# Optimization experiments

Measured on AMD Instinct MI355X. Metric: run time of the kernel, lower is better.

## Reference

```python
import jax, jax.numpy as jnp
import numpy as np

EPS = 1e-6  # VNLeakyReLU eps
NORM_EPS = 1e-12  # F.normalize default eps
NEG_SLOPE = 0.2


def _normalize(v):
    # matches torch F.normalize(p=2, dim=-1): v / max(||v||, eps)
    n = jnp.linalg.norm(v, axis=-1, keepdims=True)
    return v / jnp.maximum(n, NORM_EPS)


def _bgs_extended(d6s):
    # d6s: [B,N,D,3,2] -> rotation matrices [B,N,D,3,3] (columns b1,b2,b3)
    b1 = _normalize(d6s[..., 0])
    a2 = d6s[..., 1]
    proj = jnp.sum(b1 * a2, axis=-1, keepdims=True) * b1
    b2 = _normalize(a2 - proj)
    b3 = jnp.cross(b1, b2)
    return jnp.stack([b1, b2, b3], axis=-1)


def setup_inputs() -> dict:
    key = jax.random.key(0)
    kX, kJ, kA, kB, kC, kW = jax.random.split(key, 6)
    B, N, Din, Dout = 8, 4096, 128, 256
    return {
        "X": jax.random.normal(kX, (B, N, Din, 3), dtype=jnp.float32),
        "J": jax.random.normal(kJ, (B, N, Din, 3, 2), dtype=jnp.float32),
        "Amat": jax.random.normal(kA, (Dout, Din), dtype=jnp.float32),
        "Bmat": jax.random.normal(kB, (Dout, Din), dtype=jnp.float32),
        "Cmat": jax.random.normal(kC, (Dout, Din), dtype=jnp.float32),
        "Wdir": jax.random.normal(kW, (Dout, Dout), dtype=jnp.float32),
        "device": 0,
    }


def reference(X, J, Amat, Bmat, Cmat, Wdir, device):
    # ---- Affine_Linear_Abla_wocomplex ----
    R = _bgs_extended(J)  # [B,N,D,3,3]
    # get_rtx(k, RT, X) = sum_j R[...,j,k] * X[...,j]; stacking k=0,1,2 gives:
    a_term = jnp.einsum('bndjk,bndj->bndk', R, X)  # [B,N,D,3]
    # Y = A@a + B@a + C@a == (A+B+C)@a  (einsum 'fe,bcei->bcfi')
    Y = jnp.einsum('fe,bnei->bnfi', Amat + Bmat + Cmat, a_term)  # [B,N,F,3]
    # ---- permute(0,2,3,1) -> [B, F, 3, N] ----
    x = jnp.transpose(Y, (0, 2, 3, 1))
    # ---- VNLeakyReLU ----
    d = jnp.einsum('oc,bcin->boin', Wdir, x)
    dot = jnp.sum(x * d, axis=2, keepdims=True)
    mask = (dot >= 0).astype(x.dtype)
    d_norm_sq = jnp.sum(d * d, axis=2, keepdims=True)
    x_out = NEG_SLOPE * x + (1 - NEG_SLOPE) * (
        mask * x + (1 - mask) * (x - dot / (d_norm_sq + EPS) * d)
    )
    return x_out  # [B, F, 3, N]
```

## Files before the change

### kernel.cpp

```cpp
#include <hip/hip_runtime.h>

#define TT 16
#define NBLK 2048
#define LDA 136

typedef short s16x8 __attribute__((ext_vector_type(8)));
typedef float f32x4 __attribute__((ext_vector_type(4)));

#define SCHED_FENCE() __builtin_amdgcn_sched_barrier(0)

__device__ __forceinline__ unsigned short f2bf(float f) {
  union { float f; unsigned u; } v; v.f = f;
  unsigned r = v.u + 0x7FFFu + ((v.u >> 16) & 1u);
  return (unsigned short)(r >> 16);
}
__device__ __forceinline__ float bf2f(unsigned short h) {
  union { unsigned u; float f; } v; v.u = ((unsigned)h) << 16;
  return v.f;
}
__device__ __forceinline__ void split2(float x, unsigned short& h, unsigned short& m) {
  h = f2bf(x);
  m = f2bf(x - bf2f(h));
}

__global__ __launch_bounds__(256) void prep1_kernel(
    const float* __restrict__ A, const float* __restrict__ Bm,
    const float* __restrict__ C,
    float* __restrict__ M3f,
    unsigned short* __restrict__ M3h, unsigned short* __restrict__ M3m) {
  int tid = blockIdx.x * 256 + threadIdx.x;
  float s = A[tid] + Bm[tid] + C[tid];
  M3f[tid] = s;
  unsigned short h, m;
  split2(s, h, m);
  M3h[tid] = h; M3m[tid] = m;
}

__global__ __launch_bounds__(128) void prep2_kernel(
    const float* __restrict__ W, const float* __restrict__ M3f,
    unsigned short* __restrict__ WMh, unsigned short* __restrict__ WMm) {
  __shared__ float wrow[256];
  const int o = blockIdx.x;
  const int e = threadIdx.x;
  wrow[e]       = W[o * 256 + e];
  wrow[e + 128] = W[o * 256 + 128 + e];
  __syncthreads();
  float dot = 0.f;
  #pragma unroll 8
  for (int c = 0; c < 256; ++c) dot += wrow[c] * M3f[c * 128 + e];
  unsigned short h, m;
  split2(dot, h, m);
  WMh[o * 128 + e] = h; WMm[o * 128 + e] = m;
}

#define B1LOAD(ks) { \
  b1h[ks][0] = *(const s16x8*)(M3h + fB + (ks) * 32); \
  b1m[ks][0] = *(const s16x8*)(M3m + fB + (ks) * 32); \
  b1h[ks][1] = *(const s16x8*)(M3h + fB + 2048 + (ks) * 32); \
  b1m[ks][1] = *(const s16x8*)(M3m + fB + 2048 + (ks) * 32); }

#define WMLOAD(ks) { \
  wmh[ks][0] = *(const s16x8*)(WMh + fB + (ks) * 32); \
  wmm[ks][0] = *(const s16x8*)(WMm + fB + (ks) * 32); \
  wmh[ks][1] = *(const s16x8*)(WMh + fB + 2048 + (ks) * 32); \
  wmm[ks][1] = *(const s16x8*)(WMm + fB + 2048 + (ks) * 32); }

#define G1STEP(ks) { \
  const int e0 = (ks) * 32 + quad * 8; \
  _Pragma("unroll") \
  for (int mt = 0; mt < 3; ++mt) { \
    s16x8 ah = *(const s16x8*)(aTh + (mt * 16 + nl) * LDA + e0); \
    s16x8 am = *(const s16x8*)(aTm + (mt * 16 + nl) * LDA + e0); \
    _Pragma("unroll") \
    for (int nt = 0; nt < 2; ++nt) { \
      f32x4 a = acc1[mt][nt]; \
      a = __builtin_amdgcn_mfma_f32_16x16x32_bf16(ah, b1h[ks][nt], a, 0, 0, 0); \
      a = __builtin_amdgcn_mfma_f32_16x16x32_bf16(ah, b1m[ks][nt], a, 0, 0, 0); \
      a = __builtin_amdgcn_mfma_f32_16x16x32_bf16(am, b1h[ks][nt], a, 0, 0, 0); \
      acc1[mt][nt] = a; \
    } \
  } }

#define G2STEP(ks) { \
  const int e0 = (ks) * 32 + quad * 8; \
  _Pragma("unroll") \
  for (int mt = 0; mt < 3; ++mt) { \
    s16x8 ah = *(const s16x8*)(aTh + (mt * 16 + nl) * LDA + e0); \
    s16x8 am = *(const s16x8*)(aTm + (mt * 16 + nl) * LDA + e0); \
    _Pragma("unroll") \
    for (int nt = 0; nt < 2; ++nt) { \
      f32x4 a = acc2[mt][nt]; \
      a = __builtin_amdgcn_mfma_f32_16x16x32_bf16(ah, wmh[ks][nt], a, 0, 0, 0); \
      a = __builtin_amdgcn_mfma_f32_16x16x32_bf16(ah, wmm[ks][nt], a, 0, 0, 0); \
      a = __builtin_amdgcn_mfma_f32_16x16x32_bf16(am, wmh[ks][nt], a, 0, 0, 0); \
      acc2[mt][nt] = a; \
    } \
  } }

__global__ __launch_bounds__(512, 4) void affine_vnrelu_mfma(
    const float* __restrict__ X, const float* __restrict__ J,
    const unsigned short* __restrict__ M3h, const unsigned short* __restrict__ M3m,
    const unsigned short* __restrict__ WMh, const unsigned short* __restrict__ WMm,
    float* __restrict__ out) {
  __shared__ unsigned short smem[2 * 48 * LDA];
  unsigned short* aTh = smem;
  unsigned short* aTm = smem + 48 * LDA;

  const int tid = threadIdx.x;
  const int lane = tid & 63;
  const int w = tid >> 6;
  const int quad = lane >> 4;
  const int nl = lane & 15;
  const long g0 = (long)blockIdx.x * TT;
  const int b = (int)(g0 >> 12);
  const int n0 = (int)(g0 & 4095);
  const int f0 = w * 32;
  const int fB = (f0 + nl) * 128 + quad * 8;
  const f32x4 zz = {0.f, 0.f, 0.f, 0.f};

  s16x8 b1h[4][2], b1m[4][2];
  s16x8 wmh[4][2], wmm[4][2];
  B1LOAD(0);
  SCHED_FENCE();

  {
    int t = tid >> 5;
    int dch0 = (tid & 31) * 4;
    const float* Xp = X + ((g0 + t) * 128 + dch0) * 3;
    const float* Jp = J + ((g0 + t) * 128 + dch0) * 6;
    float xf[12], jf[24];
    #pragma unroll
    for (int q = 0; q < 3; ++q) *(float4*)(xf + 4 * q) = ((const float4*)Xp)[q];
    #pragma unroll
    for (int q = 0; q < 6; ++q) *(float4*)(jf + 4 * q) = ((const float4*)Jp)[q];

    unsigned short hs[3][4], ms[3][4];
    #pragma unroll
    for (int e = 0; e < 4; ++e) {
      float x0 = xf[3 * e], x1 = xf[3 * e + 1], x2 = xf[3 * e + 2];
      float j0 = jf[6 * e],     j1 = jf[6 * e + 1], j2 = jf[6 * e + 2];
      float j3 = jf[6 * e + 3], j4 = jf[6 * e + 4], j5 = jf[6 * e + 5];
      float c00 = j0, c01 = j2, c02 = j4;
      float a20 = j1, a21 = j3, a22 = j5;
      float nsq1 = c00 * c00 + c01 * c01 + c02 * c02;
      float inv1 = __builtin_amdgcn_rsqf(fmaxf(nsq1, 1e-24f));
      float b10 = c00 * inv1, b11 = c01 * inv1, b12 = c02 * inv1;
      float pr = b10 * a20 + b11 * a21 + b12 * a22;
      float u0 = a20 - pr * b10, u1 = a21 - pr * b11, u2 = a22 - pr * b12;
      float nsq2 = u0 * u0 + u1 * u1 + u2 * u2;
      float inv2 = __builtin_amdgcn_rsqf(fmaxf(nsq2, 1e-24f));
      float b20 = u0 * inv2, b21 = u1 * inv2, b22 = u2 * inv2;
      float b30 = b11 * b22 - b12 * b21;
      float b31 = b12 * b20 - b10 * b22;
      float b32 = b10 * b21 - b11 * b20;
      split2(b10 * x0 + b11 * x1 + b12 * x2, hs[0][e], ms[0][e]);
      split2(b20 * x0 + b21 * x1 + b22 * x2, hs[1][e], ms[1][e]);
      split2(b30 * x0 + b31 * x1 + b32 * x2, hs[2][e], ms[2][e]);
    }
    #pragma unroll
    for (int i = 0; i < 3; ++i) {
      short4 vh, vm;
      vh.x = hs[i][0]; vh.y = hs[i][1]; vh.z = hs[i][2]; vh.w = hs[i][3];
      vm.x = ms[i][0]; vm.y = ms[i][1]; vm.z = ms[i][2]; vm.w = ms[i][3];
      int ro = (i * 16 + t) * LDA + dch0;
      *(short4*)(aTh + ro) = vh;
      *(short4*)(aTm + ro) = vm;
    }
  }
  __syncthreads();

  f32x4 acc1[3][2];
  #pragma unroll
  for (int mt = 0; mt < 3; ++mt)
    #pragma unroll
    for (int nt = 0; nt < 2; ++nt) acc1[mt][nt] = zz;

  B1LOAD(1);
  SCHED_FENCE();
  G1STEP(0);
  B1LOAD(2);
  SCHED_FENCE();
  G1STEP(1);
  B1LOAD(3);
  SCHED_FENCE();
  G1STEP(2);
  WMLOAD(0); WMLOAD(1);
  SCHED_FENCE();
  G1STEP(3);

  f32x4 acc2[3][2];
  #pragma unroll
  for (int mt = 0; mt < 3; ++mt)
    #pragma unroll
    for (int nt = 0; nt < 2; ++nt) acc2[mt][nt] = zz;

  G2STEP(0);
  WMLOAD(2);
  SCHED_FENCE();
  G2STEP(1);
  WMLOAD(3);
  SCHED_FENCE();
  G2STEP(2);
  G2STEP(3);

  #pragma unroll
  for (int nt = 0; nt < 2; ++nt) {
    int f = f0 + nt * 16 + nl;
    float* ob = out + ((long)(b * 256 + f) * 3) * 4096 + n0 + quad * 4;
    float o[3][4];
    #pragma unroll
    for (int r = 0; r < 4; ++r) {
      float x0 = acc1[0][nt][r], x1 = acc1[1][nt][r], x2 = acc1[2][nt][r];
      float d0 = acc2[0][nt][r], d1 = acc2[1][nt][r], d2 = acc2[2][nt][r];
      float dot = x0 * d0 + x1 * d1 + x2 * d2;
      float dn = d0 * d0 + d1 * d1 + d2 * d2;
      float s = (dot < 0.0f) ? (0.8f * dot * __builtin_amdgcn_rcpf(dn + 1e-6f))
                             : 0.0f;
      o[0][r] = x0 - s * d0;
      o[1][r] = x1 - s * d1;
      o[2][r] = x2 - s * d2;
    }
    #pragma unroll
    for (int i = 0; i < 3; ++i)
      *(float4*)(ob + ((long)i * 4096)) = make_float4(o[i][0], o[i][1], o[i][2], o[i][3]);
  }
}

extern "C" void kernel_launch(void* const* d_in, const int* in_sizes, int n_in,
                              void* d_out, int out_size, void* d_ws, size_t ws_size,
                              hipStream_t stream) {
  const float* X = (const float*)d_in[0];
  const float* J = (const float*)d_in[1];
  const float* A = (const float*)d_in[2];
  const float* B = (const float*)d_in[3];
  const float* C = (const float*)d_in[4];
  const float* W = (const float*)d_in[5];
  unsigned short* M3h = (unsigned short*)d_ws;
  unsigned short* M3m = M3h + 128 * 256;
  unsigned short* WMh = M3m + 128 * 256;
  unsigned short* WMm = WMh + 128 * 256;
  float* M3f = (float*)(WMm + 128 * 256);
  float* out = (float*)d_out;

  prep1_kernel<<<128, 256, 0, stream>>>(A, B, C, M3f, M3h, M3m);
  prep2_kernel<<<256, 128, 0, stream>>>(W, M3f, WMh, WMm);
  affine_vnrelu_mfma<<<NBLK, 512, 0, stream>>>(
      X, J, M3h, M3m, WMh, WMm, out);
}
```

Before: 280.7 us.

## Interleave both GEMM chains per k-step and split prep2 reduction across two halves

```diff
diff --git a/kernel.cpp b/kernel.cpp
--- a/kernel.cpp
+++ b/kernel.cpp
@@ -36,21 +36,29 @@
   M3h[tid] = h; M3m[tid] = m;
 }
 
-__global__ __launch_bounds__(128) void prep2_kernel(
+__global__ __launch_bounds__(256) void prep2_kernel(
     const float* __restrict__ W, const float* __restrict__ M3f,
     unsigned short* __restrict__ WMh, unsigned short* __restrict__ WMm) {
   __shared__ float wrow[256];
+  __shared__ float part[128];
   const int o = blockIdx.x;
-  const int e = threadIdx.x;
-  wrow[e]       = W[o * 256 + e];
-  wrow[e + 128] = W[o * 256 + 128 + e];
+  const int t = threadIdx.x;
+  const int e = t & 127;
+  const int h = t >> 7;
+  wrow[t] = W[o * 256 + t];
   __syncthreads();
   float dot = 0.f;
+  const int c0 = h * 128;
   #pragma unroll 8
-  for (int c = 0; c < 256; ++c) dot += wrow[c] * M3f[c * 128 + e];
-  unsigned short h, m;
-  split2(dot, h, m);
-  WMh[o * 128 + e] = h; WMm[o * 128 + e] = m;
+  for (int c = c0; c < c0 + 128; ++c) dot += wrow[c] * M3f[c * 128 + e];
+  if (h) part[e] = dot;
+  __syncthreads();
+  if (!h) {
+    float d = dot + part[e];
+    unsigned short hh, mm;
+    split2(d, hh, mm);
+    WMh[o * 128 + e] = hh; WMm[o * 128 + e] = mm;
+  }
 }
 
 #define B1LOAD(ks) { \
@@ -65,7 +73,7 @@
   wmh[ks][1] = *(const s16x8*)(WMh + fB + 2048 + (ks) * 32); \
   wmm[ks][1] = *(const s16x8*)(WMm + fB + 2048 + (ks) * 32); }
 
-#define G1STEP(ks) { \
+#define GSTEP(ks) { \
   const int e0 = (ks) * 32 + quad * 8; \
   _Pragma("unroll") \
   for (int mt = 0; mt < 3; ++mt) { \
@@ -73,27 +81,15 @@
     s16x8 am = *(const s16x8*)(aTm + (mt * 16 + nl) * LDA + e0); \
     _Pragma("unroll") \
     for (int nt = 0; nt < 2; ++nt) { \
-      f32x4 a = acc1[mt][nt]; \
-      a = __builtin_amdgcn_mfma_f32_16x16x32_bf16(ah, b1h[ks][nt], a, 0, 0, 0); \
-      a = __builtin_amdgcn_mfma_f32_16x16x32_bf16(ah, b1m[ks][nt], a, 0, 0, 0); \
-      a = __builtin_amdgcn_mfma_f32_16x16x32_bf16(am, b1h[ks][nt], a, 0, 0, 0); \
-      acc1[mt][nt] = a; \
-    } \
-  } }
-
-#define G2STEP(ks) { \
-  const int e0 = (ks) * 32 + quad * 8; \
-  _Pragma("unroll") \
-  for (int mt = 0; mt < 3; ++mt) { \
-    s16x8 ah = *(const s16x8*)(aTh + (mt * 16 + nl) * LDA + e0); \
-    s16x8 am = *(const s16x8*)(aTm + (mt * 16 + nl) * LDA + e0); \
-    _Pragma("unroll") \
-    for (int nt = 0; nt < 2; ++nt) { \
-      f32x4 a = acc2[mt][nt]; \
-      a = __builtin_amdgcn_mfma_f32_16x16x32_bf16(ah, wmh[ks][nt], a, 0, 0, 0); \
-      a = __builtin_amdgcn_mfma_f32_16x16x32_bf16(ah, wmm[ks][nt], a, 0, 0, 0); \
-      a = __builtin_amdgcn_mfma_f32_16x16x32_bf16(am, wmh[ks][nt], a, 0, 0, 0); \
-      acc2[mt][nt] = a; \
+      f32x4 a1 = acc1[mt][nt]; \
+      f32x4 a2 = acc2[mt][nt]; \
+      a1 = __builtin_amdgcn_mfma_f32_16x16x32_bf16(ah, b1h[ks][nt], a1, 0, 0, 0); \
+      a2 = __builtin_amdgcn_mfma_f32_16x16x32_bf16(ah, wmh[ks][nt], a2, 0, 0, 0); \
+      a1 = __builtin_amdgcn_mfma_f32_16x16x32_bf16(ah, b1m[ks][nt], a1, 0, 0, 0); \
+      a2 = __builtin_amdgcn_mfma_f32_16x16x32_bf16(ah, wmm[ks][nt], a2, 0, 0, 0); \
+      a1 = __builtin_amdgcn_mfma_f32_16x16x32_bf16(am, b1h[ks][nt], a1, 0, 0, 0); \
+      a2 = __builtin_amdgcn_mfma_f32_16x16x32_bf16(am, wmh[ks][nt], a2, 0, 0, 0); \
+      acc1[mt][nt] = a1; acc2[mt][nt] = a2; \
     } \
   } }
 
@@ -120,7 +116,7 @@
 
   s16x8 b1h[4][2], b1m[4][2];
   s16x8 wmh[4][2], wmm[4][2];
-  B1LOAD(0);
+  B1LOAD(0); WMLOAD(0);
   SCHED_FENCE();
 
   {
@@ -169,39 +165,22 @@
   }
   __syncthreads();
 
-  f32x4 acc1[3][2];
+  f32x4 acc1[3][2], acc2[3][2];
   #pragma unroll
   for (int mt = 0; mt < 3; ++mt)
     #pragma unroll
-    for (int nt = 0; nt < 2; ++nt) acc1[mt][nt] = zz;
-
-  B1LOAD(1);
-  SCHED_FENCE();
-  G1STEP(0);
-  B1LOAD(2);
-  SCHED_FENCE();
-  G1STEP(1);
-  B1LOAD(3);
-  SCHED_FENCE();
-  G1STEP(2);
-  WMLOAD(0); WMLOAD(1);
-  SCHED_FENCE();
-  G1STEP(3);
-
-  f32x4 acc2[3][2];
-  #pragma unroll
-  for (int mt = 0; mt < 3; ++mt)
-    #pragma unroll
-    for (int nt = 0; nt < 2; ++nt) acc2[mt][nt] = zz;
-
-  G2STEP(0);
-  WMLOAD(2);
-  SCHED_FENCE();
-  G2STEP(1);
-  WMLOAD(3);
-  SCHED_FENCE();
-  G2STEP(2);
-  G2STEP(3);
+    for (int nt = 0; nt < 2; ++nt) { acc1[mt][nt] = zz; acc2[mt][nt] = zz; }
+
+  B1LOAD(1); WMLOAD(1);
+  SCHED_FENCE();
+  GSTEP(0);
+  B1LOAD(2); WMLOAD(2);
+  SCHED_FENCE();
+  GSTEP(1);
+  B1LOAD(3); WMLOAD(3);
+  SCHED_FENCE();
+  GSTEP(2);
+  GSTEP(3);
 
   #pragma unroll
   for (int nt = 0; nt < 2; ++nt) {
@@ -243,7 +222,7 @@
   float* out = (float*)d_out;
 
   prep1_kernel<<<128, 256, 0, stream>>>(A, B, C, M3f, M3h, M3m);
-  prep2_kernel<<<256, 128, 0, stream>>>(W, M3f, WMh, WMm);
+  prep2_kernel<<<256, 256, 0, stream>>>(W, M3f, WMh, WMm);
   affine_vnrelu_mfma<<<NBLK, 512, 0, stream>>>(
       X, J, M3h, M3m, WMh, WMm, out);
 }
```

Result: slower. 298.0 us (+6.2%).
